# Performance work log

Hardware: AMD Instinct MI355X
Metric: run time of the kernel (lower is better)

The kernel has to match this reference:

```python
import jax, jax.numpy as jnp
import numpy as np

D_MODEL = 1024
H = 16
D_K = D_MODEL // H


def setup_inputs() -> dict:
    key = jax.random.key(0)
    ks = jax.random.split(key, 12)
    B, S = 4, 2048
    q = jax.random.normal(ks[0], (B, S, D_MODEL), jnp.float32)
    k = jax.random.normal(ks[1], (B, S, D_MODEL), jnp.float32)
    v = jax.random.normal(ks[2], (B, S, D_MODEL), jnp.float32)
    # causal mask, broadcastable to [B, H, S, S]; mask==0 positions are blocked
    mask = jnp.tril(jnp.ones((S, S), jnp.int32))[None, None]
    scale = 1.0 / np.sqrt(D_MODEL)
    Wq = jax.random.normal(ks[3], (D_MODEL, D_MODEL), jnp.float32) * scale
    bq = jax.random.normal(ks[4], (D_MODEL,), jnp.float32) * 0.02
    Wk = jax.random.normal(ks[5], (D_MODEL, D_MODEL), jnp.float32) * scale
    bk = jax.random.normal(ks[6], (D_MODEL,), jnp.float32) * 0.02
    Wv = jax.random.normal(ks[7], (D_MODEL, D_MODEL), jnp.float32) * scale
    bv = jax.random.normal(ks[8], (D_MODEL,), jnp.float32) * 0.02
    Wo = jax.random.normal(ks[9], (D_MODEL, D_MODEL), jnp.float32) * scale
    bo = jax.random.normal(ks[10], (D_MODEL,), jnp.float32) * 0.02
    return {"q": q, "k": k, "v": v, "mask": mask,
            "Wq": Wq, "bq": bq, "Wk": Wk, "bk": bk,
            "Wv": Wv, "bv": bv, "Wo": Wo, "bo": bo}


def reference(q, k, v, mask, Wq, bq, Wk, bk, Wv, bv, Wo, bo):
    B, S, _ = q.shape
    # linear projections (torch nn.Linear: x @ W.T + b)
    query = q @ Wq.T + bq
    key = k @ Wk.T + bk
    value = v @ Wv.T + bv
    # [B, S, D] -> [B, H, S, d_k]
    def split_heads(x):
        return x.reshape(B, S, H, D_K).transpose(0, 2, 1, 3)
    query, key, value = split_heads(query), split_heads(key), split_heads(value)
    # scaled dot-product attention, scores: [B, H, S, S]
    scores = jnp.einsum('bhqd,bhkd->bhqk', query, key) / np.sqrt(D_K)
    scores = jnp.where(mask == 0, jnp.float32(-1e9), scores)
    attn = jax.nn.softmax(scores, axis=-1)
    x = jnp.einsum('bhqk,bhkd->bhqd', attn, value)  # [B, H, S, d_k]
    x = x.transpose(0, 2, 1, 3).reshape(B, S, D_MODEL)
    return x @ Wo.T + bo
```

## Files before the change

kernel.cpp:

```cpp
#include <hip/hip_runtime.h>

#define DM 1024
#define SEQ 2048
#define NH 16
#define DK 64

typedef __bf16 bf16x8 __attribute__((ext_vector_type(8)));
typedef float f32x4 __attribute__((ext_vector_type(4)));

#define QSCALE 0.1803368801111244f

__device__ inline unsigned short f2bf(float f) {
    unsigned u = __float_as_uint(f);
    u += 0x7fffu + ((u >> 16) & 1u);
    return (unsigned short)(u >> 16);
}

__device__ inline unsigned pkbf(float lo, float hi) {
    union { __bf16 h[2]; unsigned u; } r;
    r.h[0] = (__bf16)lo; r.h[1] = (__bf16)hi;
    return r.u;
}

__global__ __launch_bounds__(256) void cvt_w(const float* __restrict__ s0,
                                             const float* __restrict__ s1,
                                             const float* __restrict__ s2,
                                             const float* __restrict__ s3,
                                             unsigned short* __restrict__ d0,
                                             unsigned short* __restrict__ d1,
                                             unsigned short* __restrict__ d2,
                                             unsigned short* __restrict__ d3) {
    const float* s;
    unsigned short* d;
    switch (blockIdx.y) {
        case 0: s = s0; d = d0; break;
        case 1: s = s1; d = d1; break;
        case 2: s = s2; d = d2; break;
        default: s = s3; d = d3; break;
    }
    int i = (blockIdx.x * 256 + threadIdx.x) * 4;
    float4 v = *(const float4*)(s + i);
    ushort4 o;
    o.x = f2bf(v.x); o.y = f2bf(v.y); o.z = f2bf(v.z); o.w = f2bf(v.w);
    *(ushort4*)(d + i) = o;
}

template <bool A_BF16, int OUT_MODE>
__global__ __launch_bounds__(512) void gemm_bt(const void* __restrict__ Av,
                                               const unsigned short* __restrict__ W,
                                               const float* __restrict__ bias,
                                               void* __restrict__ Cv,
                                               float oscale) {
    __shared__ unsigned short lds_a[2][128 * 64];
    __shared__ unsigned short lds_w[2][128 * 64];

    const int K = DM, N = DM;
    const int t = threadIdx.x;
    const int lane = t & 63;
    const int w = t >> 6;
    const int wr = w >> 1;
    const int wc = w & 1;
    const int bid = blockIdx.x;
    const int xcd = bid & 7;
    const int idx = bid >> 3;
    const int rowBase = (xcd * 8 + (idx >> 3)) * 128;
    const int colBase = (idx & 7) * 128;
    const int l15 = lane & 15;
    const int lg = lane >> 4;
    const int ar = t >> 2, aq = t & 3;
    const int NIT = K >> 6;

    f32x4 acc[2][4] = {};

    auto STAGE_W = [&](int kt, int buf) {
#pragma unroll
        for (int i = 0; i < 2; ++i) {
            const int row = (w * 2 + i) * 8 + (lane >> 3);
            const int sl = lane & 7;
            const unsigned short* src =
                W + (size_t)(colBase + row) * K + kt * 64 + ((sl ^ (row & 7)) * 8);
            __builtin_amdgcn_global_load_lds(src, &lds_w[buf][(w * 2 + i) * 512], 16, 0, 0);
        }
    };
    auto STAGE_A16 = [&](int kt, int buf) {
#pragma unroll
        for (int i = 0; i < 2; ++i) {
            const int row = (w * 2 + i) * 8 + (lane >> 3);
            const int sl = lane & 7;
            const unsigned short* src = (const unsigned short*)Av +
                (size_t)(rowBase + row) * K + kt * 64 + ((sl ^ (row & 7)) * 8);
            __builtin_amdgcn_global_load_lds(src, &lds_a[buf][(w * 2 + i) * 512], 16, 0, 0);
        }
    };
    auto LOADA = [&](int kt, float4* rf) {
        const float* Af = (const float*)Av + (size_t)(rowBase + ar) * K + kt * 64 + aq * 16;
#pragma unroll
        for (int i = 0; i < 4; ++i) rf[i] = *(const float4*)(Af + i * 4);
    };
    auto WRITEA = [&](const float4* rf, int buf) {
#pragma unroll
        for (int i = 0; i < 2; ++i) {
            union { __bf16 h[8]; uint4 u; } pk;
            pk.h[0] = (__bf16)rf[2 * i].x; pk.h[1] = (__bf16)rf[2 * i].y;
            pk.h[2] = (__bf16)rf[2 * i].z; pk.h[3] = (__bf16)rf[2 * i].w;
            pk.h[4] = (__bf16)rf[2 * i + 1].x; pk.h[5] = (__bf16)rf[2 * i + 1].y;
            pk.h[6] = (__bf16)rf[2 * i + 1].z; pk.h[7] = (__bf16)rf[2 * i + 1].w;
            *(uint4*)&lds_a[buf][ar * 64 + (((aq * 2 + i) ^ (ar & 7)) * 8)] = pk.u;
        }
    };
    auto COMPUTE = [&](int buf) {
#pragma unroll
        for (int kh = 0; kh < 2; ++kh) {
            bf16x8 af[2], wf[4];
#pragma unroll
            for (int m = 0; m < 2; ++m)
                af[m] = *(const bf16x8*)&lds_a[buf][(wr * 32 + m * 16 + l15) * 64 +
                                                   (((kh * 4 + lg) ^ (l15 & 7)) * 8)];
#pragma unroll
            for (int n = 0; n < 4; ++n)
                wf[n] = *(const bf16x8*)&lds_w[buf][(wc * 64 + n * 16 + l15) * 64 +
                                                   (((kh * 4 + lg) ^ (l15 & 7)) * 8)];
#pragma unroll
            for (int m = 0; m < 2; ++m)
#pragma unroll
                for (int n = 0; n < 4; ++n)
                    acc[m][n] = __builtin_amdgcn_mfma_f32_16x16x32_bf16(af[m], wf[n],
                                                                        acc[m][n], 0, 0, 0);
        }
    };

    if (A_BF16) {
        STAGE_W(0, 0);
        STAGE_A16(0, 0);
        for (int kt = 0; kt < NIT; ++kt) {
            const int cur = kt & 1;
            if (kt + 1 < NIT) {
                STAGE_W(kt + 1, cur ^ 1);
                STAGE_A16(kt + 1, cur ^ 1);
                asm volatile("s_waitcnt vmcnt(4)" ::: "memory");
            } else {
                asm volatile("s_waitcnt vmcnt(0)" ::: "memory");
            }
            __builtin_amdgcn_s_barrier();
            COMPUTE(cur);
            __builtin_amdgcn_s_barrier();
        }
    } else {
        float4 ra[4], rb[4];
        STAGE_W(0, 0);
        LOADA(0, ra);
        for (int kt = 0; kt < NIT; kt += 2) {
            if (kt + 1 < NIT) {
                STAGE_W(kt + 1, 1);
                LOADA(kt + 1, rb);
                asm volatile("s_waitcnt vmcnt(6)" ::: "memory");
            } else {
                asm volatile("s_waitcnt vmcnt(0)" ::: "memory");
            }
            WRITEA(ra, 0);
            asm volatile("s_waitcnt lgkmcnt(0)" ::: "memory");
            __builtin_amdgcn_s_barrier();
            COMPUTE(0);
            __builtin_amdgcn_s_barrier();
            if (kt + 2 < NIT) {
                STAGE_W(kt + 2, 0);
                LOADA(kt + 2, ra);
                asm volatile("s_waitcnt vmcnt(6)" ::: "memory");
            } else {
                asm volatile("s_waitcnt vmcnt(0)" ::: "memory");
            }
            WRITEA(rb, 1);
            asm volatile("s_waitcnt lgkmcnt(0)" ::: "memory");
            __builtin_amdgcn_s_barrier();
            COMPUTE(1);
            __builtin_amdgcn_s_barrier();
        }
    }

#pragma unroll
    for (int m = 0; m < 2; ++m) {
        int row = rowBase + wr * 32 + m * 16 + lg * 4;
#pragma unroll
        for (int n = 0; n < 4; ++n) {
            int col = colBase + wc * 64 + n * 16 + l15;
            float bv = bias[col];
            if (OUT_MODE == 2) {
                const int bh = (row >> 11) * NH + (col >> 6);
                const int dloc = col & 63;
                const int s = row & (SEQ - 1);
                ushort4 o;
                o.x = f2bf(acc[m][n][0] + bv);
                o.y = f2bf(acc[m][n][1] + bv);
                o.z = f2bf(acc[m][n][2] + bv);
                o.w = f2bf(acc[m][n][3] + bv);
                *(ushort4*)((unsigned short*)Cv + ((size_t)bh * DK + dloc) * SEQ + s) = o;
            } else if (OUT_MODE == 1) {
#pragma unroll
                for (int j = 0; j < 4; ++j)
                    ((float*)Cv)[(size_t)(row + j) * N + col] = acc[m][n][j] + bv;
            } else {
#pragma unroll
                for (int j = 0; j < 4; ++j)
                    ((unsigned short*)Cv)[(size_t)(row + j) * N + col] =
                        f2bf((acc[m][n][j] + bv) * oscale);
            }
        }
    }
}

__global__ __launch_bounds__(256) void attn(const unsigned short* __restrict__ Q,
                                            const unsigned short* __restrict__ K,
                                            const unsigned short* __restrict__ Vt,
                                            unsigned short* __restrict__ X) {
    __shared__ unsigned short k_lds[2][64 * 64];
    __shared__ unsigned short v_lds[2][64 * 64];

    const int t = threadIdx.x;
    const int lane = t & 63;
    const int w = t >> 6;
    const int l15 = lane & 15, lg = lane >> 4;
    const int c4 = (lane >> 4) & 1, c5 = (lane >> 5) & 1;

    const int orig = blockIdx.x;
    const int flat = (orig & 7) * 128 + (orig >> 3);
    const int bh = flat >> 4;
    const int pr = flat & 15;
    const int b = bh >> 4, h = bh & 15;

    const unsigned short* Qb = Q + (size_t)b * SEQ * DM + h * DK;
    const unsigned short* Kb = K + (size_t)b * SEQ * DM + h * DK;
    const unsigned short* Vb = Vt + (size_t)bh * DK * SEQ;

    const int sr = t >> 3;
    const int sc8 = (t & 7) * 8;
    const int sxo = (sr & 7) * 8;
    const int xork = (l15 & 7) * 8;

    union { unsigned short us[8]; bf16x8 v; } ou;
#pragma unroll
    for (int i = 0; i < 8; ++i) ou.us[i] = 0x3F80;
    const bf16x8 onesf = ou.v;

    bf16x8 kr0, kr1, vr0, vr1;
    int gp = 0;

    auto LOADT = [&](int kv0) {
        kr0 = *(const bf16x8*)(Kb + (size_t)(kv0 + sr) * DM + sc8);
        kr1 = *(const bf16x8*)(Kb + (size_t)(kv0 + 32 + sr) * DM + sc8);
        vr0 = *(const bf16x8*)(Vb + (size_t)sr * SEQ + kv0 + sc8);
        vr1 = *(const bf16x8*)(Vb + (size_t)(32 + sr) * SEQ + kv0 + sc8);
    };

    LOADT(0);

    for (int task = 0; task < 2; ++task) {
        const int qt = task ? 31 - pr : pr;
        const int qrow0 = qt * 64 + w * 16;
        const int qg = qrow0 + l15;

        const bf16x8 qf0 = *(const bf16x8*)(Qb + (size_t)(qrow0 + l15) * DM + lg * 8);
        const bf16x8 qf1 = *(const bf16x8*)(Qb + (size_t)(qrow0 + l15) * DM + lg * 8 + 32);

        f32x4 acc[4] = {};
        f32x4 accS = {};
        const int nt = qt + 1;

        for (int tile = 0; tile < nt; ++tile) {
            const int kv0 = tile << 6;
            unsigned short* kl = k_lds[gp & 1];
            unsigned short* vl = v_lds[gp & 1];
            *(bf16x8*)&kl[sr * 64 + (sc8 ^ sxo)] = kr0;
            *(bf16x8*)&kl[(sr + 32) * 64 + (sc8 ^ sxo)] = kr1;
            *(bf16x8*)&vl[sr * 64 + (sc8 ^ sxo)] = vr0;
            *(bf16x8*)&vl[(sr + 32) * 64 + (sc8 ^ sxo)] = vr1;
            __syncthreads();

            if (tile + 1 < nt)
                LOADT((tile + 1) << 6);
            else if (task == 0)
                LOADT(0);

            f32x4 st[4];
#pragma unroll
            for (int s = 0; s < 4; ++s) {
                const int rb2 = (s * 16 + l15) * 64;
                bf16x8 ka = *(const bf16x8*)&kl[rb2 + ((lg * 8) ^ xork)];
                bf16x8 kb2 = *(const bf16x8*)&kl[rb2 + ((32 + lg * 8) ^ xork)];
                f32x4 z = {};
                z = __builtin_amdgcn_mfma_f32_16x16x32_bf16(ka, qf0, z, 0, 0, 0);
                st[s] = __builtin_amdgcn_mfma_f32_16x16x32_bf16(kb2, qf1, z, 0, 0, 0);
            }

            bf16x8 vf[4][2];
#pragma unroll
            for (int d = 0; d < 4; ++d) {
                const int rb2 = (d * 16 + l15) * 64;
                vf[d][0] = *(const bf16x8*)&vl[rb2 + ((lg * 8) ^ xork)];
                vf[d][1] = *(const bf16x8*)&vl[rb2 + ((32 + lg * 8) ^ xork)];
            }

            float ps[16];
            if (kv0 + 63 > qrow0) {
#pragma unroll
                for (int s = 0; s < 4; ++s)
#pragma unroll
                    for (int j = 0; j < 4; ++j) {
                        const bool ok = kv0 + s * 16 + 4 * lg + j <= qg;
                        ps[s * 4 + j] = ok ? exp2f(fminf(st[s][j], 30.0f)) : 0.0f;
                    }
            } else {
#pragma unroll
                for (int s = 0; s < 4; ++s)
#pragma unroll
                    for (int j = 0; j < 4; ++j)
                        ps[s * 4 + j] = exp2f(fminf(st[s][j], 30.0f));
            }

            bf16x8 pf[2];
#pragma unroll
            for (int hh = 0; hh < 2; ++hh) {
                const float* p8 = &ps[hh * 8];
                unsigned wsp[2][2];
#pragma unroll
                for (int s = 0; s < 2; ++s)
#pragma unroll
                    for (int p2 = 0; p2 < 2; ++p2)
                        wsp[s][p2] = pkbf(p8[s * 4 + 2 * p2], p8[s * 4 + 2 * p2 + 1]);
                unsigned n0[2], n1[2];
#pragma unroll
                for (int p2 = 0; p2 < 2; ++p2) {
                    unsigned snd = c5 ? wsp[0][p2] : wsp[1][p2];
                    unsigned exch = __shfl_xor((int)snd, 32, 64);
                    n0[p2] = c5 ? exch : wsp[0][p2];
                    n1[p2] = c5 ? wsp[1][p2] : exch;
                }
                unsigned f0[2], f1[2];
#pragma unroll
                for (int p2 = 0; p2 < 2; ++p2) {
                    unsigned snd = c4 ? n0[p2] : n1[p2];
                    unsigned exch = __shfl_xor((int)snd, 16, 64);
                    f0[p2] = c4 ? exch : n0[p2];
                    f1[p2] = c4 ? n1[p2] : exch;
                }
                union { unsigned u[4]; bf16x8 v; } pu;
                pu.u[0] = f0[0]; pu.u[1] = f0[1]; pu.u[2] = f1[0]; pu.u[3] = f1[1];
                pf[hh] = pu.v;
            }

#pragma unroll
            for (int d = 0; d < 4; ++d) {
                acc[d] = __builtin_amdgcn_mfma_f32_16x16x32_bf16(vf[d][0], pf[0], acc[d], 0, 0, 0);
                acc[d] = __builtin_amdgcn_mfma_f32_16x16x32_bf16(vf[d][1], pf[1], acc[d], 0, 0, 0);
            }
            accS = __builtin_amdgcn_mfma_f32_16x16x32_bf16(onesf, pf[0], accS, 0, 0, 0);
            accS = __builtin_amdgcn_mfma_f32_16x16x32_bf16(onesf, pf[1], accS, 0, 0, 0);
            gp++;
        }

        const float inv = 1.0f / accS[0];
#pragma unroll
        for (int d = 0; d < 4; ++d) {
            ushort4 o;
            o.x = f2bf(acc[d][0] * inv);
            o.y = f2bf(acc[d][1] * inv);
            o.z = f2bf(acc[d][2] * inv);
            o.w = f2bf(acc[d][3] * inv);
            *(ushort4*)&X[(size_t)(b * SEQ + qg) * DM + h * DK + d * 16 + 4 * lg] = o;
        }
    }
}

extern "C" void kernel_launch(void* const* d_in, const int* in_sizes, int n_in,
                              void* d_out, int out_size, void* d_ws, size_t ws_size,
                              hipStream_t stream) {
    const float* q  = (const float*)d_in[0];
    const float* k  = (const float*)d_in[1];
    const float* v  = (const float*)d_in[2];
    const float* Wq = (const float*)d_in[4];
    const float* bq = (const float*)d_in[5];
    const float* Wk = (const float*)d_in[6];
    const float* bk = (const float*)d_in[7];
    const float* Wv = (const float*)d_in[8];
    const float* bv = (const float*)d_in[9];
    const float* Wo = (const float*)d_in[10];
    const float* bo = (const float*)d_in[11];

    const size_t NEL = (size_t)4 * SEQ * DM;
    const size_t WEL = (size_t)DM * DM;
    unsigned short* Qp  = (unsigned short*)d_ws;
    unsigned short* Kp  = Qp + NEL;
    unsigned short* Vp  = Kp + NEL;
    unsigned short* Vt  = Vp + NEL;
    unsigned short* Wob = Vt + NEL;
    unsigned short* Xp  = Vp;
    unsigned short* Wqb = (unsigned short*)d_out;
    unsigned short* Wkb = Wqb + WEL;
    unsigned short* Wvb = Wkb + WEL;

    hipLaunchKernelGGL(cvt_w, dim3(1024, 4), dim3(256), 0, stream, Wq, Wk, Wv, Wo,
                       Wqb, Wkb, Wvb, Wob);
    hipLaunchKernelGGL((gemm_bt<false, 0>), dim3(512), dim3(512), 0, stream,
                       (const void*)q, Wqb, bq, (void*)Qp, QSCALE);
    hipLaunchKernelGGL((gemm_bt<false, 0>), dim3(512), dim3(512), 0, stream,
                       (const void*)k, Wkb, bk, (void*)Kp, 1.0f);
    hipLaunchKernelGGL((gemm_bt<false, 2>), dim3(512), dim3(512), 0, stream,
                       (const void*)v, Wvb, bv, (void*)Vt, 1.0f);
    hipLaunchKernelGGL(attn, dim3(1024), dim3(256), 0, stream, Qp, Kp, Vt, Xp);
    hipLaunchKernelGGL((gemm_bt<true, 1>), dim3(512), dim3(512), 0, stream,
                       (const void*)Xp, Wob, bo, d_out, 1.0f);
}
```

Measured before the change: 216.5 us.

## Double attention KV tile to 128 rows and split GEMM into separate kernels

The attention kernel now stages 128 keys/values per LDS tile instead of 64, using a new V swizzle. It processes each tile as two 64-wide halves and skips the causally-masked second half, which halves the number of barriers and tile iterations per query tile. The templated GEMM is split into a projection kernel that takes fp32 A through a single A LDS buffer with a runtime out_mode, and a separate bf16 output-projection kernel. The exp2 clamp at 30 is removed. The larger tiles raise LDS use and register pressure, which may lower occupancy.

```diff
diff --git a/kernel.cpp b/kernel.cpp
--- a/kernel.cpp
+++ b/kernel.cpp
@@ -45,13 +45,12 @@
     *(ushort4*)(d + i) = o;
 }
 
-template <bool A_BF16, int OUT_MODE>
-__global__ __launch_bounds__(512) void gemm_bt(const void* __restrict__ Av,
-                                               const unsigned short* __restrict__ W,
-                                               const float* __restrict__ bias,
-                                               void* __restrict__ Cv,
-                                               float oscale) {
-    __shared__ unsigned short lds_a[2][128 * 64];
+__global__ __launch_bounds__(512) void gemm_proj(const float* __restrict__ A,
+                                                 const unsigned short* __restrict__ W,
+                                                 const float* __restrict__ bias,
+                                                 unsigned short* __restrict__ C,
+                                                 float oscale, int out_mode) {
+    __shared__ unsigned short lds_a[128 * 64];
     __shared__ unsigned short lds_w[2][128 * 64];
 
     const int K = DM, N = DM;
@@ -82,22 +81,12 @@
             __builtin_amdgcn_global_load_lds(src, &lds_w[buf][(w * 2 + i) * 512], 16, 0, 0);
         }
     };
-    auto STAGE_A16 = [&](int kt, int buf) {
-#pragma unroll
-        for (int i = 0; i < 2; ++i) {
-            const int row = (w * 2 + i) * 8 + (lane >> 3);
-            const int sl = lane & 7;
-            const unsigned short* src = (const unsigned short*)Av +
-                (size_t)(rowBase + row) * K + kt * 64 + ((sl ^ (row & 7)) * 8);
-            __builtin_amdgcn_global_load_lds(src, &lds_a[buf][(w * 2 + i) * 512], 16, 0, 0);
-        }
-    };
     auto LOADA = [&](int kt, float4* rf) {
-        const float* Af = (const float*)Av + (size_t)(rowBase + ar) * K + kt * 64 + aq * 16;
+        const float* Af = A + (size_t)(rowBase + ar) * K + kt * 64 + aq * 16;
 #pragma unroll
         for (int i = 0; i < 4; ++i) rf[i] = *(const float4*)(Af + i * 4);
     };
-    auto WRITEA = [&](const float4* rf, int buf) {
+    auto WRITEA = [&](const float4* rf) {
 #pragma unroll
         for (int i = 0; i < 2; ++i) {
             union { __bf16 h[8]; uint4 u; } pk;
@@ -105,21 +94,21 @@
             pk.h[2] = (__bf16)rf[2 * i].z; pk.h[3] = (__bf16)rf[2 * i].w;
             pk.h[4] = (__bf16)rf[2 * i + 1].x; pk.h[5] = (__bf16)rf[2 * i + 1].y;
             pk.h[6] = (__bf16)rf[2 * i + 1].z; pk.h[7] = (__bf16)rf[2 * i + 1].w;
-            *(uint4*)&lds_a[buf][ar * 64 + (((aq * 2 + i) ^ (ar & 7)) * 8)] = pk.u;
-        }
-    };
-    auto COMPUTE = [&](int buf) {
+            *(uint4*)&lds_a[ar * 64 + (((aq * 2 + i) ^ (ar & 7)) * 8)] = pk.u;
+        }
+    };
+    auto COMPUTE = [&](int wbuf) {
 #pragma unroll
         for (int kh = 0; kh < 2; ++kh) {
             bf16x8 af[2], wf[4];
 #pragma unroll
             for (int m = 0; m < 2; ++m)
-                af[m] = *(const bf16x8*)&lds_a[buf][(wr * 32 + m * 16 + l15) * 64 +
-                                                   (((kh * 4 + lg) ^ (l15 & 7)) * 8)];
+                af[m] = *(const bf16x8*)&lds_a[(wr * 32 + m * 16 + l15) * 64 +
+                                               (((kh * 4 + lg) ^ (l15 & 7)) * 8)];
 #pragma unroll
             for (int n = 0; n < 4; ++n)
-                wf[n] = *(const bf16x8*)&lds_w[buf][(wc * 64 + n * 16 + l15) * 64 +
-                                                   (((kh * 4 + lg) ^ (l15 & 7)) * 8)];
+                wf[n] = *(const bf16x8*)&lds_w[wbuf][(wc * 64 + n * 16 + l15) * 64 +
+                                                    (((kh * 4 + lg) ^ (l15 & 7)) * 8)];
 #pragma unroll
             for (int m = 0; m < 2; ++m)
 #pragma unroll
@@ -129,52 +118,34 @@
         }
     };
 
-    if (A_BF16) {
-        STAGE_W(0, 0);
-        STAGE_A16(0, 0);
-        for (int kt = 0; kt < NIT; ++kt) {
-            const int cur = kt & 1;
-            if (kt + 1 < NIT) {
-                STAGE_W(kt + 1, cur ^ 1);
-                STAGE_A16(kt + 1, cur ^ 1);
-                asm volatile("s_waitcnt vmcnt(4)" ::: "memory");
-            } else {
-                asm volatile("s_waitcnt vmcnt(0)" ::: "memory");
-            }
-            __builtin_amdgcn_s_barrier();
-            COMPUTE(cur);
-            __builtin_amdgcn_s_barrier();
-        }
-    } else {
-        float4 ra[4], rb[4];
-        STAGE_W(0, 0);
-        LOADA(0, ra);
-        for (int kt = 0; kt < NIT; kt += 2) {
-            if (kt + 1 < NIT) {
-                STAGE_W(kt + 1, 1);
-                LOADA(kt + 1, rb);
-                asm volatile("s_waitcnt vmcnt(6)" ::: "memory");
-            } else {
-                asm volatile("s_waitcnt vmcnt(0)" ::: "memory");
-            }
-            WRITEA(ra, 0);
-            asm volatile("s_waitcnt lgkmcnt(0)" ::: "memory");
-            __builtin_amdgcn_s_barrier();
-            COMPUTE(0);
-            __builtin_amdgcn_s_barrier();
-            if (kt + 2 < NIT) {
-                STAGE_W(kt + 2, 0);
-                LOADA(kt + 2, ra);
-                asm volatile("s_waitcnt vmcnt(6)" ::: "memory");
-            } else {
-                asm volatile("s_waitcnt vmcnt(0)" ::: "memory");
-            }
-            WRITEA(rb, 1);
-            asm volatile("s_waitcnt lgkmcnt(0)" ::: "memory");
-            __builtin_amdgcn_s_barrier();
-            COMPUTE(1);
-            __builtin_amdgcn_s_barrier();
-        }
+    float4 ra[4], rb[4];
+    STAGE_W(0, 0);
+    LOADA(0, ra);
+    for (int kt = 0; kt < NIT; kt += 2) {
+        if (kt + 1 < NIT) {
+            STAGE_W(kt + 1, 1);
+            LOADA(kt + 1, rb);
+            asm volatile("s_waitcnt vmcnt(6)" ::: "memory");
+        } else {
+            asm volatile("s_waitcnt vmcnt(0)" ::: "memory");
+        }
+        WRITEA(ra);
+        asm volatile("s_waitcnt lgkmcnt(0)" ::: "memory");
+        __builtin_amdgcn_s_barrier();
+        COMPUTE(0);
+        __builtin_amdgcn_s_barrier();
+        if (kt + 2 < NIT) {
+            STAGE_W(kt + 2, 0);
+            LOADA(kt + 2, ra);
+            asm volatile("s_waitcnt vmcnt(6)" ::: "memory");
+        } else {
+            asm volatile("s_waitcnt vmcnt(0)" ::: "memory");
+        }
+        WRITEA(rb);
+        asm volatile("s_waitcnt lgkmcnt(0)" ::: "memory");
+        __builtin_amdgcn_s_barrier();
+        COMPUTE(1);
+        __builtin_amdgcn_s_barrier();
     }
 
 #pragma unroll
@@ -184,7 +155,7 @@
         for (int n = 0; n < 4; ++n) {
             int col = colBase + wc * 64 + n * 16 + l15;
             float bv = bias[col];
-            if (OUT_MODE == 2) {
+            if (out_mode == 2) {
                 const int bh = (row >> 11) * NH + (col >> 6);
                 const int dloc = col & 63;
                 const int s = row & (SEQ - 1);
@@ -193,17 +164,99 @@
                 o.y = f2bf(acc[m][n][1] + bv);
                 o.z = f2bf(acc[m][n][2] + bv);
                 o.w = f2bf(acc[m][n][3] + bv);
-                *(ushort4*)((unsigned short*)Cv + ((size_t)bh * DK + dloc) * SEQ + s) = o;
-            } else if (OUT_MODE == 1) {
+                *(ushort4*)(C + ((size_t)bh * DK + dloc) * SEQ + s) = o;
+            } else {
 #pragma unroll
                 for (int j = 0; j < 4; ++j)
-                    ((float*)Cv)[(size_t)(row + j) * N + col] = acc[m][n][j] + bv;
-            } else {
-#pragma unroll
-                for (int j = 0; j < 4; ++j)
-                    ((unsigned short*)Cv)[(size_t)(row + j) * N + col] =
-                        f2bf((acc[m][n][j] + bv) * oscale);
+                    C[(size_t)(row + j) * N + col] = f2bf((acc[m][n][j] + bv) * oscale);
             }
+        }
+    }
+}
+
+__global__ __launch_bounds__(512) void gemm_out(const unsigned short* __restrict__ A,
+                                                const unsigned short* __restrict__ W,
+                                                const float* __restrict__ bias,
+                                                float* __restrict__ C) {
+    __shared__ unsigned short lds_a[2][128 * 64];
+    __shared__ unsigned short lds_w[2][128 * 64];
+
+    const int K = DM, N = DM;
+    const int t = threadIdx.x;
+    const int lane = t & 63;
+    const int w = t >> 6;
+    const int wr = w >> 1;
+    const int wc = w & 1;
+    const int bid = blockIdx.x;
+    const int xcd = bid & 7;
+    const int idx = bid >> 3;
+    const int rowBase = (xcd * 8 + (idx >> 3)) * 128;
+    const int colBase = (idx & 7) * 128;
+    const int l15 = lane & 15;
+    const int lg = lane >> 4;
+    const int NIT = K >> 6;
+
+    f32x4 acc[2][4] = {};
+
+    auto STAGE = [&](const unsigned short* M0, unsigned short* ldsb, int kt) {
+#pragma unroll
+        for (int i = 0; i < 2; ++i) {
+            const int row = (w * 2 + i) * 8 + (lane >> 3);
+            const int sl = lane & 7;
+            const unsigned short* src =
+                M0 + (size_t)row * K + kt * 64 + ((sl ^ (row & 7)) * 8);
+            __builtin_amdgcn_global_load_lds(src, ldsb + (w * 2 + i) * 512, 16, 0, 0);
+        }
+    };
+    auto COMPUTE = [&](int buf) {
+#pragma unroll
+        for (int kh = 0; kh < 2; ++kh) {
+            bf16x8 af[2], wf[4];
+#pragma unroll
+            for (int m = 0; m < 2; ++m)
+                af[m] = *(const bf16x8*)&lds_a[buf][(wr * 32 + m * 16 + l15) * 64 +
+                                                   (((kh * 4 + lg) ^ (l15 & 7)) * 8)];
+#pragma unroll
+            for (int n = 0; n < 4; ++n)
+                wf[n] = *(const bf16x8*)&lds_w[buf][(wc * 64 + n * 16 + l15) * 64 +
+                                                   (((kh * 4 + lg) ^ (l15 & 7)) * 8)];
+#pragma unroll
+            for (int m = 0; m < 2; ++m)
+#pragma unroll
+                for (int n = 0; n < 4; ++n)
+                    acc[m][n] = __builtin_amdgcn_mfma_f32_16x16x32_bf16(af[m], wf[n],
+                                                                        acc[m][n], 0, 0, 0);
+        }
+    };
+
+    const unsigned short* Arow = A + (size_t)rowBase * K;
+    const unsigned short* Wrow = W + (size_t)colBase * K;
+    STAGE(Wrow, lds_w[0], 0);
+    STAGE(Arow, lds_a[0], 0);
+    for (int kt = 0; kt < NIT; ++kt) {
+        const int cur = kt & 1;
+        if (kt + 1 < NIT) {
+            STAGE(Wrow, lds_w[cur ^ 1], kt + 1);
+            STAGE(Arow, lds_a[cur ^ 1], kt + 1);
+            asm volatile("s_waitcnt vmcnt(4)" ::: "memory");
+        } else {
+            asm volatile("s_waitcnt vmcnt(0)" ::: "memory");
+        }
+        __builtin_amdgcn_s_barrier();
+        COMPUTE(cur);
+        __builtin_amdgcn_s_barrier();
+    }
+
+#pragma unroll
+    for (int m = 0; m < 2; ++m) {
+        int row = rowBase + wr * 32 + m * 16 + lg * 4;
+#pragma unroll
+        for (int n = 0; n < 4; ++n) {
+            int col = colBase + wc * 64 + n * 16 + l15;
+            float bv = bias[col];
+#pragma unroll
+            for (int j = 0; j < 4; ++j)
+                C[(size_t)(row + j) * N + col] = acc[m][n][j] + bv;
         }
     }
 }
@@ -212,8 +265,8 @@
                                             const unsigned short* __restrict__ K,
                                             const unsigned short* __restrict__ Vt,
                                             unsigned short* __restrict__ X) {
-    __shared__ unsigned short k_lds[2][64 * 64];
-    __shared__ unsigned short v_lds[2][64 * 64];
+    __shared__ unsigned short k_lds[2][128 * 64];
+    __shared__ unsigned short v_lds[2][64 * 128];
 
     const int t = threadIdx.x;
     const int lane = t & 63;
@@ -231,9 +284,12 @@
     const unsigned short* Kb = K + (size_t)b * SEQ * DM + h * DK;
     const unsigned short* Vb = Vt + (size_t)bh * DK * SEQ;
 
-    const int sr = t >> 3;
-    const int sc8 = (t & 7) * 8;
-    const int sxo = (sr & 7) * 8;
+    const int ksr = t >> 3;
+    const int ksc8 = (t & 7) * 8;
+    const int kxo = (ksr & 7) * 8;
+    const int vsr = t >> 2;
+    const int vq = t & 3;
+    const int vxo = vsr & 15;
     const int xork = (l15 & 7) * 8;
 
     union { unsigned short us[8]; bf16x8 v; } ou;
@@ -241,14 +297,16 @@
     for (int i = 0; i < 8; ++i) ou.us[i] = 0x3F80;
     const bf16x8 onesf = ou.v;
 
-    bf16x8 kr0, kr1, vr0, vr1;
+    bf16x8 kr[4], vr[4];
     int gp = 0;
 
     auto LOADT = [&](int kv0) {
-        kr0 = *(const bf16x8*)(Kb + (size_t)(kv0 + sr) * DM + sc8);
-        kr1 = *(const bf16x8*)(Kb + (size_t)(kv0 + 32 + sr) * DM + sc8);
-        vr0 = *(const bf16x8*)(Vb + (size_t)sr * SEQ + kv0 + sc8);
-        vr1 = *(const bf16x8*)(Vb + (size_t)(32 + sr) * SEQ + kv0 + sc8);
+#pragma unroll
+        for (int i = 0; i < 4; ++i)
+            kr[i] = *(const bf16x8*)(Kb + (size_t)(kv0 + i * 32 + ksr) * DM + ksc8);
+#pragma unroll
+        for (int j = 0; j < 4; ++j)
+            vr[j] = *(const bf16x8*)(Vb + (size_t)vsr * SEQ + kv0 + (j * 4 + vq) * 8);
     };
 
     LOADT(0);
@@ -263,97 +321,105 @@
 
         f32x4 acc[4] = {};
         f32x4 accS = {};
-        const int nt = qt + 1;
+        const int nt = (qt + 2) >> 1;
 
         for (int tile = 0; tile < nt; ++tile) {
-            const int kv0 = tile << 6;
+            const int kv0 = tile << 7;
             unsigned short* kl = k_lds[gp & 1];
             unsigned short* vl = v_lds[gp & 1];
-            *(bf16x8*)&kl[sr * 64 + (sc8 ^ sxo)] = kr0;
-            *(bf16x8*)&kl[(sr + 32) * 64 + (sc8 ^ sxo)] = kr1;
-            *(bf16x8*)&vl[sr * 64 + (sc8 ^ sxo)] = vr0;
-            *(bf16x8*)&vl[(sr + 32) * 64 + (sc8 ^ sxo)] = vr1;
+#pragma unroll
+            for (int i = 0; i < 4; ++i)
+                *(bf16x8*)&kl[(i * 32 + ksr) * 64 + (ksc8 ^ kxo)] = kr[i];
+#pragma unroll
+            for (int j = 0; j < 4; ++j)
+                *(bf16x8*)&vl[vsr * 128 + (((j * 4 + vq) ^ vxo) * 8)] = vr[j];
             __syncthreads();
 
             if (tile + 1 < nt)
-                LOADT((tile + 1) << 6);
+                LOADT((tile + 1) << 7);
             else if (task == 0)
                 LOADT(0);
 
-            f32x4 st[4];
-#pragma unroll
-            for (int s = 0; s < 4; ++s) {
-                const int rb2 = (s * 16 + l15) * 64;
-                bf16x8 ka = *(const bf16x8*)&kl[rb2 + ((lg * 8) ^ xork)];
-                bf16x8 kb2 = *(const bf16x8*)&kl[rb2 + ((32 + lg * 8) ^ xork)];
-                f32x4 z = {};
-                z = __builtin_amdgcn_mfma_f32_16x16x32_bf16(ka, qf0, z, 0, 0, 0);
-                st[s] = __builtin_amdgcn_mfma_f32_16x16x32_bf16(kb2, qf1, z, 0, 0, 0);
+#pragma unroll
+            for (int hh = 0; hh < 2; ++hh) {
+                const int kvb = kv0 + hh * 64;
+                if (kvb > qrow0 + 15) break;
+
+                f32x4 st[4];
+#pragma unroll
+                for (int s = 0; s < 4; ++s) {
+                    const int rb2 = (hh * 64 + s * 16 + l15) * 64;
+                    bf16x8 ka = *(const bf16x8*)&kl[rb2 + ((lg * 8) ^ xork)];
+                    bf16x8 kb2 = *(const bf16x8*)&kl[rb2 + ((32 + lg * 8) ^ xork)];
+                    f32x4 z = {};
+                    z = __builtin_amdgcn_mfma_f32_16x16x32_bf16(ka, qf0, z, 0, 0, 0);
+                    st[s] = __builtin_amdgcn_mfma_f32_16x16x32_bf16(kb2, qf1, z, 0, 0, 0);
+                }
+
+                bf16x8 vf[4][2];
+#pragma unroll
+                for (int d = 0; d < 4; ++d) {
+                    const int base = (d * 16 + l15) * 128;
+                    vf[d][0] = *(const bf16x8*)&vl[base + (((hh * 8 + lg) ^ l15) * 8)];
+                    vf[d][1] = *(const bf16x8*)&vl[base + (((hh * 8 + 4 + lg) ^ l15) * 8)];
+                }
+
+                float ps[16];
+                if (kvb + 63 > qrow0) {
+#pragma unroll
+                    for (int s = 0; s < 4; ++s)
+#pragma unroll
+                        for (int j = 0; j < 4; ++j) {
+                            const bool ok = kvb + s * 16 + 4 * lg + j <= qg;
+                            ps[s * 4 + j] = ok ? exp2f(st[s][j]) : 0.0f;
+                        }
+                } else {
+#pragma unroll
+                    for (int s = 0; s < 4; ++s)
+#pragma unroll
+                        for (int j = 0; j < 4; ++j)
+                            ps[s * 4 + j] = exp2f(st[s][j]);
+                }
+
+                bf16x8 pf[2];
+#pragma unroll
+                for (int hq = 0; hq < 2; ++hq) {
+                    const float* p8 = &ps[hq * 8];
+                    unsigned wsp[2][2];
+#pragma unroll
+                    for (int s = 0; s < 2; ++s)
+#pragma unroll
+                        for (int p2 = 0; p2 < 2; ++p2)
+                            wsp[s][p2] = pkbf(p8[s * 4 + 2 * p2], p8[s * 4 + 2 * p2 + 1]);
+                    unsigned n0[2], n1[2];
+#pragma unroll
+                    for (int p2 = 0; p2 < 2; ++p2) {
+                        unsigned snd = c5 ? wsp[0][p2] : wsp[1][p2];
+                        unsigned exch = __shfl_xor((int)snd, 32, 64);
+                        n0[p2] = c5 ? exch : wsp[0][p2];
+                        n1[p2] = c5 ? wsp[1][p2] : exch;
+                    }
+                    unsigned f0[2], f1[2];
+#pragma unroll
+                    for (int p2 = 0; p2 < 2; ++p2) {
+                        unsigned snd = c4 ? n0[p2] : n1[p2];
+                        unsigned exch = __shfl_xor((int)snd, 16, 64);
+                        f0[p2] = c4 ? exch : n0[p2];
+                        f1[p2] = c4 ? n1[p2] : exch;
+                    }
+                    union { unsigned u[4]; bf16x8 v; } pu;
+                    pu.u[0] = f0[0]; pu.u[1] = f0[1]; pu.u[2] = f1[0]; pu.u[3] = f1[1];
+                    pf[hq] = pu.v;
+                }
+
+#pragma unroll
+                for (int d = 0; d < 4; ++d) {
+                    acc[d] = __builtin_amdgcn_mfma_f32_16x16x32_bf16(vf[d][0], pf[0], acc[d], 0, 0, 0);
+                    acc[d] = __builtin_amdgcn_mfma_f32_16x16x32_bf16(vf[d][1], pf[1], acc[d], 0, 0, 0);
+                }
+                accS = __builtin_amdgcn_mfma_f32_16x16x32_bf16(onesf, pf[0], accS, 0, 0, 0);
+                accS = __builtin_amdgcn_mfma_f32_16x16x32_bf16(onesf, pf[1], accS, 0, 0, 0);
             }
-
-            bf16x8 vf[4][2];
-#pragma unroll
-            for (int d = 0; d < 4; ++d) {
-                const int rb2 = (d * 16 + l15) * 64;
-                vf[d][0] = *(const bf16x8*)&vl[rb2 + ((lg * 8) ^ xork)];
-                vf[d][1] = *(const bf16x8*)&vl[rb2 + ((32 + lg * 8) ^ xork)];
-            }
-
-            float ps[16];
-            if (kv0 + 63 > qrow0) {
-#pragma unroll
-                for (int s = 0; s < 4; ++s)
-#pragma unroll
-                    for (int j = 0; j < 4; ++j) {
-                        const bool ok = kv0 + s * 16 + 4 * lg + j <= qg;
-                        ps[s * 4 + j] = ok ? exp2f(fminf(st[s][j], 30.0f)) : 0.0f;
-                    }
-            } else {
-#pragma unroll
-                for (int s = 0; s < 4; ++s)
-#pragma unroll
-                    for (int j = 0; j < 4; ++j)
-                        ps[s * 4 + j] = exp2f(fminf(st[s][j], 30.0f));
-            }
-
-            bf16x8 pf[2];
-#pragma unroll
-            for (int hh = 0; hh < 2; ++hh) {
-                const float* p8 = &ps[hh * 8];
-                unsigned wsp[2][2];
-#pragma unroll
-                for (int s = 0; s < 2; ++s)
-#pragma unroll
-                    for (int p2 = 0; p2 < 2; ++p2)
-                        wsp[s][p2] = pkbf(p8[s * 4 + 2 * p2], p8[s * 4 + 2 * p2 + 1]);
-                unsigned n0[2], n1[2];
-#pragma unroll
-                for (int p2 = 0; p2 < 2; ++p2) {
-                    unsigned snd = c5 ? wsp[0][p2] : wsp[1][p2];
-                    unsigned exch = __shfl_xor((int)snd, 32, 64);
-                    n0[p2] = c5 ? exch : wsp[0][p2];
-                    n1[p2] = c5 ? wsp[1][p2] : exch;
-                }
-                unsigned f0[2], f1[2];
-#pragma unroll
-                for (int p2 = 0; p2 < 2; ++p2) {
-                    unsigned snd = c4 ? n0[p2] : n1[p2];
-                    unsigned exch = __shfl_xor((int)snd, 16, 64);
-                    f0[p2] = c4 ? exch : n0[p2];
-                    f1[p2] = c4 ? n1[p2] : exch;
-                }
-                union { unsigned u[4]; bf16x8 v; } pu;
-                pu.u[0] = f0[0]; pu.u[1] = f0[1]; pu.u[2] = f1[0]; pu.u[3] = f1[1];
-                pf[hh] = pu.v;
-            }
-
-#pragma unroll
-            for (int d = 0; d < 4; ++d) {
-                acc[d] = __builtin_amdgcn_mfma_f32_16x16x32_bf16(vf[d][0], pf[0], acc[d], 0, 0, 0);
-                acc[d] = __builtin_amdgcn_mfma_f32_16x16x32_bf16(vf[d][1], pf[1], acc[d], 0, 0, 0);
-            }
-            accS = __builtin_amdgcn_mfma_f32_16x16x32_bf16(onesf, pf[0], accS, 0, 0, 0);
-            accS = __builtin_amdgcn_mfma_f32_16x16x32_bf16(onesf, pf[1], accS, 0, 0, 0);
             gp++;
         }
 
@@ -399,13 +465,13 @@
 
     hipLaunchKernelGGL(cvt_w, dim3(1024, 4), dim3(256), 0, stream, Wq, Wk, Wv, Wo,
                        Wqb, Wkb, Wvb, Wob);
-    hipLaunchKernelGGL((gemm_bt<false, 0>), dim3(512), dim3(512), 0, stream,
-                       (const void*)q, Wqb, bq, (void*)Qp, QSCALE);
-    hipLaunchKernelGGL((gemm_bt<false, 0>), dim3(512), dim3(512), 0, stream,
-                       (const void*)k, Wkb, bk, (void*)Kp, 1.0f);
-    hipLaunchKernelGGL((gemm_bt<false, 2>), dim3(512), dim3(512), 0, stream,
-                       (const void*)v, Wvb, bv, (void*)Vt, 1.0f);
+    hipLaunchKernelGGL(gemm_proj, dim3(512), dim3(512), 0, stream, q, Wqb, bq, Qp,
+                       QSCALE, 0);
+    hipLaunchKernelGGL(gemm_proj, dim3(512), dim3(512), 0, stream, k, Wkb, bk, Kp,
+                       1.0f, 0);
+    hipLaunchKernelGGL(gemm_proj, dim3(512), dim3(512), 0, stream, v, Wvb, bv, Vt,
+                       1.0f, 2);
     hipLaunchKernelGGL(attn, dim3(1024), dim3(256), 0, stream, Qp, Kp, Vt, Xp);
-    hipLaunchKernelGGL((gemm_bt<true, 1>), dim3(512), dim3(512), 0, stream,
-                       (const void*)Xp, Wob, bo, d_out, 1.0f);
-}
+    hipLaunchKernelGGL(gemm_out, dim3(512), dim3(512), 0, stream, Xp, Wob, bo,
+                       (float*)d_out);
+}
```

New measurement: 223.2 us. 1.03x slower.
